# Kernel optimization log

Measured on AMD Instinct MI355X. Metric: run time of the kernel, lower is better.

Reference implementation:

```python
import jax, jax.numpy as jnp
import numpy as np

B, C, H, W = 4, 256, 64, 64
C8 = C // 8
MH, MW = 256, 256  # mask input resolution


def _conv(x, w, b, pad, dil=1):
    out = jax.lax.conv_general_dilated(
        x, w, window_strides=(1, 1),
        padding=[(pad, pad), (pad, pad)],
        rhs_dilation=(dil, dil),
        dimension_numbers=("NCHW", "OIHW", "NCHW"))
    return out + b[None, :, None, None]


def setup_inputs() -> dict:
    key = jax.random.key(0)
    ks = jax.random.split(key, 16)

    def w_init(k, shape):
        fan_in = shape[1] * shape[2] * shape[3]
        bound = 1.0 / np.sqrt(fan_in)
        return jax.random.uniform(k, shape, jnp.float32, -bound, bound)

    def b_init(k, n, fan_in):
        bound = 1.0 / np.sqrt(fan_in)
        return jax.random.uniform(k, (n,), jnp.float32, -bound, bound)

    return {
        "x": jax.random.normal(ks[0], (B, C, H, W), jnp.float32),
        "mask": jax.random.uniform(ks[1], (B, 1, MH, MW), jnp.float32),
        "w_ctx": w_init(ks[2], (C, C, 7, 7)),   "b_ctx": b_init(ks[3], C, C * 49),
        "w_wide": w_init(ks[4], (C, C, 5, 5)),  "b_wide": b_init(ks[5], C, C * 25),
        "w_comb": w_init(ks[6], (C, 2 * C, 1, 1)), "b_comb": b_init(ks[7], C, 2 * C),
        "w_q": w_init(ks[8], (C8, C, 1, 1)),    "b_q": b_init(ks[9], C8, C),
        "w_k": w_init(ks[10], (C8, C, 1, 1)),   "b_k": b_init(ks[11], C8, C),
        "w_v": w_init(ks[12], (C, C, 1, 1)),    "b_v": b_init(ks[13], C, C),
    }


def reference(x, mask, w_ctx, b_ctx, w_wide, b_wide, w_comb, b_comb,
              w_q, b_q, w_k, b_k, w_v, b_v):
    local_ctx = _conv(x, w_ctx, b_ctx, pad=3, dil=1)          # [B,C,H,W]
    wide_ctx = _conv(x, w_wide, b_wide, pad=6, dil=3)         # [B,C,H,W]
    multi = _conv(jnp.concatenate([local_ctx, wide_ctx], axis=1),
                  w_comb, b_comb, pad=0)                       # [B,C,H,W]

    b, c, h, w = multi.shape
    n = h * w
    q = _conv(multi, w_q, b_q, pad=0).reshape(b, C8, n)        # [B,C/8,N]
    k = _conv(multi, w_k, b_k, pad=0).reshape(b, C8, n)        # [B,C/8,N]
    v = _conv(multi, w_v, b_v, pad=0).reshape(b, c, n)         # [B,C,N]

    scores = jnp.einsum("bcm,bcn->bmn", q, k)                  # [B,N,N]
    attn = jax.nn.softmax(scores, axis=-1)
    out = jnp.einsum("bcn,bmn->bcm", v, attn).reshape(b, c, h, w)

    # nearest-neighbor resize of mask to (h, w), matching torch F.interpolate
    mh, mw = mask.shape[2], mask.shape[3]
    idx_h = (jnp.arange(h) * mh) // h
    idx_w = (jnp.arange(w) * mw) // w
    mask_r = mask[:, :, idx_h][:, :, :, idx_w]                 # [B,1,h,w]

    return out * (1.0 + mask_r)
```

## Files before the change

kernel.cpp:

```cpp
#include <hip/hip_runtime.h>
#include <math.h>

#define BB 4
#define CC 256
#define HH 64
#define WW 64
#define NN 4096

typedef _Float16 f16x8 __attribute__((ext_vector_type(8)));
typedef float f32x4 __attribute__((ext_vector_type(4)));

__global__ __launch_bounds__(256) void pad_kernel(
    const float* __restrict__ x, _Float16* __restrict__ xpad)
{
  int blk = blockIdx.x;
  int pr = blk % 76;
  int b  = blk / 76;
  int ci = threadIdx.x;
  int r = pr - 6;
  _Float16* dst = xpad + (((size_t)b*76 + pr)*76)*256 + ci;
  if (r < 0 || r >= HH) {
    for (int pc = 0; pc < 76; ++pc) dst[(size_t)pc*256] = (_Float16)0.f;
  } else {
    const float* src = x + ((size_t)b*CC + ci)*NN + (size_t)r*WW;
    for (int pc = 0; pc < 76; ++pc) {
      int c = pc - 6;
      float v = (c >= 0 && c < WW) ? src[c] : 0.f;
      dst[(size_t)pc*256] = (_Float16)v;
    }
  }
}

__global__ __launch_bounds__(256) void wcvt_kernel(
    const float* __restrict__ src, _Float16* __restrict__ dst, int T)
{
  int co = blockIdx.x;
  int ci = threadIdx.x;
  const float* s = src + ((size_t)co*256 + ci)*T;
  for (int t = 0; t < T; ++t)
    dst[(size_t)t*65536 + co*256 + ci] = (_Float16)s[t];
}

__global__ __launch_bounds__(256) void fcvt_kernel(
    const float* __restrict__ src, _Float16* __restrict__ dst, int n)
{
  int i = blockIdx.x * 256 + threadIdx.x;
  if (i < n) dst[i] = (_Float16)src[i];
}

template<int KS, int DIL>
__device__ __forceinline__ void conv_body(
    int blk, const _Float16* __restrict__ xpad, const _Float16* __restrict__ wb,
    const float* __restrict__ bias, _Float16* __restrict__ ctx_t, int c_off,
    char* xs)
{
  int ytile = blk & 31;
  int cot = (blk >> 5) & 1;
  int b = blk >> 6;
  int y0 = ytile * 2;
  int tid = threadIdx.x;
  int lane = tid & 63;
  int wv = tid >> 6;
  int wco = wv >> 1;
  int wsp = wv & 1;
  int l15 = lane & 15;
  int lg  = lane >> 4;

  f32x4 acc[2][4];
  #pragma unroll
  for (int m = 0; m < 2; ++m)
    #pragma unroll
    for (int n = 0; n < 4; ++n) acc[m][n] = (f32x4){0.f, 0.f, 0.f, 0.f};

  for (int kh = 0; kh < KS; ++kh) {
    int prow = 6 + y0 + (kh - KS/2) * DIL;
    const uint4* src = (const uint4*)(xpad + (((size_t)b*76 + prow)*76)*256);
    __syncthreads();
    #pragma unroll
    for (int i = 0; i < 10; ++i) {
      int ch = tid + i*512;
      if (ch < 4864) {
        uint4 v = src[ch];
        int r = ch >> 5, cq = ch & 31;
        *(uint4*)(xs + r*512 + ((cq << 4) ^ ((r & 7) << 4))) = v;
      }
    }
    __syncthreads();
    for (int kw = 0; kw < KS; ++kw) {
      int dx = (kw - KS/2) * DIL;
      int tap = kh*KS + kw;
      const _Float16* wt = wb + ((size_t)tap << 16)
                              + ((size_t)(cot*128 + wco*32 + l15) << 8) + (lg << 3);
      #pragma unroll
      for (int half = 0; half < 2; ++half) {
        f16x8 w0[4], w1[4];
        #pragma unroll
        for (int kq = 0; kq < 4; ++kq) {
          int ks = half*4 + kq;
          w0[kq] = *(const f16x8*)(wt + ks*32);
          w1[kq] = *(const f16x8*)(wt + 16*256 + ks*32);
        }
        #pragma unroll
        for (int kq = 0; kq < 4; ++kq) {
          int ks = half*4 + kq;
          #pragma unroll
          for (int nf = 0; nf < 4; ++nf) {
            int r = wsp*76 + 6 + nf*16 + l15 + dx;
            f16x8 bf = *(const f16x8*)(xs + r*512 + ((ks*64 + (lg << 4)) ^ ((r & 7) << 4)));
            acc[0][nf] = __builtin_amdgcn_mfma_f32_16x16x32_f16(w0[kq], bf, acc[0][nf], 0, 0, 0);
            acc[1][nf] = __builtin_amdgcn_mfma_f32_16x16x32_f16(w1[kq], bf, acc[1][nf], 0, 0, 0);
          }
        }
      }
    }
  }

  __syncthreads();
  _Float16* ep = (_Float16*)xs;
  #pragma unroll
  for (int m = 0; m < 2; ++m)
    #pragma unroll
    for (int i = 0; i < 4; ++i) {
      int co_l = wco*32 + m*16 + lg*4 + i;
      float bs = bias[cot*128 + co_l];
      #pragma unroll
      for (int nf = 0; nf < 4; ++nf) {
        int n_l = wsp*64 + nf*16 + l15;
        ep[n_l*136 + co_l] = (_Float16)(acc[m][nf][i] + bs);
      }
    }
  __syncthreads();
  const int cbase = c_off + cot*128;
  #pragma unroll
  for (int it = 0; it < 4; ++it) {
    int idx = tid + it*512;
    int n_l = idx >> 4, q = idx & 15;
    f16x8 val = *(const f16x8*)(ep + n_l*136 + q*8);
    *(f16x8*)(ctx_t + ((size_t)b*4096 + (size_t)y0*64 + n_l)*512 + cbase + q*8) = val;
  }
}

__global__ __launch_bounds__(512, 4) void conv_both_kernel(
    const _Float16* __restrict__ xpad,
    const _Float16* __restrict__ wb7, const _Float16* __restrict__ wb5,
    const float* __restrict__ b7, const float* __restrict__ b5,
    _Float16* __restrict__ ctx_t)
{
  __shared__ __align__(16) char xs[2*76*512];
  if (blockIdx.x < 256)
    conv_body<7, 1>(blockIdx.x, xpad, wb7, b7, ctx_t, 0, xs);
  else
    conv_body<5, 3>(blockIdx.x - 256, xpad, wb5, b5, ctx_t, 256, xs);
}

template<int K, int O, int BIASMODE>
__global__ __launch_bounds__(64) void gemm_nmajor_kernel(
    const _Float16* __restrict__ A, const _Float16* __restrict__ Wt,
    const float* __restrict__ bias0, const float* __restrict__ bias1,
    _Float16* __restrict__ outh)
{
  int nt = blockIdx.x;
  int ot = blockIdx.y;
  int lane = threadIdx.x;
  int l15 = lane & 15, lg = lane >> 4;
  int n0 = nt*64, o0 = ot*64;
  f32x4 acc[4][4] = {};
  for (int k0 = 0; k0 < K; k0 += 32) {
    f16x8 a[4], bfr[4];
    #pragma unroll
    for (int f = 0; f < 4; ++f)
      a[f] = *(const f16x8*)(A + (size_t)(n0 + f*16 + l15)*K + k0 + lg*8);
    #pragma unroll
    for (int f = 0; f < 4; ++f)
      bfr[f] = *(const f16x8*)(Wt + (size_t)(o0 + f*16 + l15)*K + k0 + lg*8);
    #pragma unroll
    for (int i = 0; i < 4; ++i)
      #pragma unroll
      for (int j = 0; j < 4; ++j)
        acc[i][j] = __builtin_amdgcn_mfma_f32_16x16x32_f16(a[i], bfr[j], acc[i][j], 0, 0, 0);
  }
  #pragma unroll
  for (int i = 0; i < 4; ++i)
    #pragma unroll
    for (int j = 0; j < 4; ++j)
      #pragma unroll
      for (int r = 0; r < 4; ++r) {
        int n = n0 + i*16 + lg*4 + r;
        int o = o0 + j*16 + l15;
        float bs = (BIASMODE == 0) ? bias0[o] : (o < 32 ? bias0[o] : bias1[o - 32]);
        outh[(size_t)n*O + o] = (_Float16)(acc[i][j][r] + bs);
      }
}

__global__ __launch_bounds__(64) void gemm_v_kernel(
    const _Float16* __restrict__ M, const _Float16* __restrict__ Wv,
    const float* __restrict__ bias, _Float16* __restrict__ v)
{
  int nt = blockIdx.x;
  int ct = blockIdx.y;
  int lane = threadIdx.x;
  int l15 = lane & 15, lg = lane >> 4;
  int n0 = nt*64, c0 = ct*64;
  f32x4 acc[4][4] = {};
  for (int k0 = 0; k0 < 256; k0 += 32) {
    f16x8 a[4], bfr[4];
    #pragma unroll
    for (int f = 0; f < 4; ++f)
      a[f] = *(const f16x8*)(Wv + (size_t)(c0 + f*16 + l15)*256 + k0 + lg*8);
    #pragma unroll
    for (int f = 0; f < 4; ++f)
      bfr[f] = *(const f16x8*)(M + (size_t)(n0 + f*16 + l15)*256 + k0 + lg*8);
    #pragma unroll
    for (int i = 0; i < 4; ++i)
      #pragma unroll
      for (int j = 0; j < 4; ++j)
        acc[i][j] = __builtin_amdgcn_mfma_f32_16x16x32_f16(a[i], bfr[j], acc[i][j], 0, 0, 0);
  }
  #pragma unroll
  for (int i = 0; i < 4; ++i)
    #pragma unroll
    for (int j = 0; j < 4; ++j)
      #pragma unroll
      for (int r = 0; r < 4; ++r) {
        int c = c0 + i*16 + lg*4 + r;
        int n_abs = n0 + j*16 + l15;
        int b = n_abs >> 12, n = n_abs & 4095;
        v[((size_t)(b*256 + c))*4096 + n] = (_Float16)(acc[i][j][r] + bias[c]);
      }
}

__global__ __launch_bounds__(256) void attn_stats_kernel(
    const _Float16* __restrict__ qh,
    float* __restrict__ rowmaxP, float* __restrict__ rowsumP)
{
  int blk = blockIdx.x;
  int b = blk >> 7, mt = (blk >> 1) & 63, nh = blk & 1;
  int tid = threadIdx.x, lane = tid & 63, w = tid >> 6;
  int l15 = lane & 15, lg = lane >> 4;
  size_t bN = (size_t)b * 4096;
  int mrow = mt*64 + w*16;
  f16x8 ah = *(const f16x8*)(qh + (bN + mrow + l15)*64 + lg*8);
  float rm[4] = {-3e38f, -3e38f, -3e38f, -3e38f};
  float sm[4] = {0.f, 0.f, 0.f, 0.f};
  for (int n0 = nh*2048; n0 < nh*2048 + 2048; n0 += 16) {
    f16x8 bh = *(const f16x8*)(qh + (bN + n0 + l15)*64 + 32 + lg*8);
    f32x4 s = {};
    s = __builtin_amdgcn_mfma_f32_16x16x32_f16(ah, bh, s, 0, 0, 0);
    #pragma unroll
    for (int i = 0; i < 4; ++i) {
      float nm = fmaxf(rm[i], s[i]);
      sm[i] = sm[i]*__expf(rm[i] - nm) + __expf(s[i] - nm);
      rm[i] = nm;
    }
  }
  #pragma unroll
  for (int off = 1; off <= 8; off <<= 1) {
    #pragma unroll
    for (int i = 0; i < 4; ++i) {
      float rmo = __shfl_xor(rm[i], off);
      float smo = __shfl_xor(sm[i], off);
      float M = fmaxf(rm[i], rmo);
      sm[i] = sm[i]*__expf(rm[i] - M) + smo*__expf(rmo - M);
      rm[i] = M;
    }
  }
  if (l15 == 0) {
    #pragma unroll
    for (int i = 0; i < 4; ++i) {
      size_t idx = (size_t)nh*16384 + bN + mrow + lg*4 + i;
      rowmaxP[idx] = rm[i];
      rowsumP[idx] = sm[i];
    }
  }
}

__global__ __launch_bounds__(512) void attn_out_kernel(
    const _Float16* __restrict__ qh, const _Float16* __restrict__ v,
    const float* __restrict__ rowmaxP, const float* __restrict__ rowsumP,
    const float* __restrict__ mask, float* __restrict__ out)
{
  __shared__ union U {
    struct { __align__(16) _Float16 vs[256*40]; __align__(16) _Float16 pl[64*40]; } s;
    float epi[256*68];
  } u;
  int blk = blockIdx.x;
  int b = blk >> 6, mt = blk & 63;
  int tid = threadIdx.x, lane = tid & 63, w = tid >> 6;
  int l15 = lane & 15, lg = lane >> 4;
  size_t bN = (size_t)b * 4096;
  int m0 = mt*64;

  int mf = w >> 1, nf2 = w & 1;
  f16x8 ah = *(const f16x8*)(qh + (bN + m0 + mf*16 + l15)*64 + lg*8);
  float rm[4], rsi[4];
  #pragma unroll
  for (int i = 0; i < 4; ++i) {
    size_t m = bN + m0 + mf*16 + lg*4 + i;
    float r0 = rowmaxP[m], r1 = rowmaxP[16384 + m];
    float s0 = rowsumP[m], s1 = rowsumP[16384 + m];
    float M = fmaxf(r0, r1);
    rm[i] = M;
    rsi[i] = 1.0f / (s0*__expf(r0 - M) + s1*__expf(r1 - M));
  }
  int mh = w >> 2, cw = (w & 3)*64;
  f32x4 acc[2][4] = {};
  const _Float16* vb = v + (size_t)b*256*4096;

  for (int n0 = 0; n0 < 4096; n0 += 32) {
    #pragma unroll
    for (int it = 0; it < 2; ++it) {
      int idx = tid + it*512;
      int c = idx >> 2, q = idx & 3;
      *(f16x8*)(u.s.vs + c*40 + q*8) = *(const f16x8*)(vb + (size_t)c*4096 + n0 + q*8);
    }
    {
      f16x8 bh = *(const f16x8*)(qh + (bN + n0 + nf2*16 + l15)*64 + 32 + lg*8);
      f32x4 s = {};
      s = __builtin_amdgcn_mfma_f32_16x16x32_f16(ah, bh, s, 0, 0, 0);
      #pragma unroll
      for (int i = 0; i < 4; ++i) {
        float p = __expf(s[i] - rm[i]) * rsi[i];
        u.s.pl[(mf*16 + lg*4 + i)*40 + nf2*16 + l15] = (_Float16)p;
      }
    }
    __syncthreads();
    {
      f16x8 pa[2], pb[4];
      #pragma unroll
      for (int af = 0; af < 2; ++af)
        pa[af] = *(const f16x8*)(u.s.pl + (mh*32 + af*16 + l15)*40 + lg*8);
      #pragma unroll
      for (int bf = 0; bf < 4; ++bf)
        pb[bf] = *(const f16x8*)(u.s.vs + (cw + bf*16 + l15)*40 + lg*8);
      #pragma unroll
      for (int af = 0; af < 2; ++af)
        #pragma unroll
        for (int bf = 0; bf < 4; ++bf)
          acc[af][bf] = __builtin_amdgcn_mfma_f32_16x16x32_f16(pa[af], pb[bf], acc[af][bf], 0, 0, 0);
    }
    __syncthreads();
  }

  #pragma unroll
  for (int af = 0; af < 2; ++af)
    #pragma unroll
    for (int bf = 0; bf < 4; ++bf)
      #pragma unroll
      for (int r = 0; r < 4; ++r) {
        int c = cw + bf*16 + l15;
        int ml = mh*32 + af*16 + lg*4 + r;
        u.epi[c*68 + ml] = acc[af][bf][r];
      }
  __syncthreads();
  const float* mb = mask + (size_t)b*65536 + (size_t)(mt*4)*256;
  #pragma unroll
  for (int it = 0; it < 8; ++it) {
    int idx = tid + it*512;
    int c = idx >> 4, q = idx & 15;
    f32x4 val = *(const f32x4*)(u.epi + c*68 + q*4);
    f32x4 o4;
    #pragma unroll
    for (int jj = 0; jj < 4; ++jj) {
      int xcol = q*4 + jj;
      o4[jj] = val[jj] * (1.0f + mb[xcol*4]);
    }
    *(f32x4*)(out + ((size_t)b*256 + c)*4096 + m0 + q*4) = o4;
  }
}

extern "C" void kernel_launch(void* const* d_in, const int* in_sizes, int n_in,
                              void* d_out, int out_size, void* d_ws, size_t ws_size,
                              hipStream_t stream)
{
  (void)in_sizes; (void)n_in; (void)out_size; (void)ws_size;
  const float* x      = (const float*)d_in[0];
  const float* mask   = (const float*)d_in[1];
  const float* w_ctx  = (const float*)d_in[2];
  const float* b_ctx  = (const float*)d_in[3];
  const float* w_wide = (const float*)d_in[4];
  const float* b_wide = (const float*)d_in[5];
  const float* w_comb = (const float*)d_in[6];
  const float* b_comb = (const float*)d_in[7];
  const float* w_q    = (const float*)d_in[8];
  const float* b_q    = (const float*)d_in[9];
  const float* w_k    = (const float*)d_in[10];
  const float* b_k    = (const float*)d_in[11];
  const float* w_v    = (const float*)d_in[12];
  const float* b_v    = (const float*)d_in[13];
  float* out = (float*)d_out;

  float* ws = (float*)d_ws;
  _Float16* xpad    = (_Float16*)(ws);
  _Float16* wb7     = (_Float16*)(ws + 2957312);
  _Float16* wb5     = (_Float16*)(ws + 4562944);
  _Float16* ctx_t   = (_Float16*)(ws + 5382144);
  _Float16* wcombH  = (_Float16*)(ws + 9576448);
  _Float16* wqkH    = (_Float16*)(ws + 9641984);
  _Float16* wvH     = (_Float16*)(ws + 9650176);
  _Float16* multi_t = (_Float16*)(ws);
  _Float16* qkt_h   = (_Float16*)(ws + 2097152);
  float*    rowmaxP = ws + 2621440;
  float*    rowsumP = ws + 2654208;
  _Float16* vbuf    = (_Float16*)(ws + 5382144);

  pad_kernel<<<BB*76, 256, 0, stream>>>(x, xpad);
  wcvt_kernel<<<256, 256, 0, stream>>>(w_ctx, wb7, 49);
  wcvt_kernel<<<256, 256, 0, stream>>>(w_wide, wb5, 25);
  fcvt_kernel<<<512, 256, 0, stream>>>(w_comb, wcombH, 131072);
  fcvt_kernel<<<32, 256, 0, stream>>>(w_q, wqkH, 8192);
  fcvt_kernel<<<32, 256, 0, stream>>>(w_k, wqkH + 8192, 8192);
  fcvt_kernel<<<256, 256, 0, stream>>>(w_v, wvH, 65536);

  conv_both_kernel<<<512, 512, 0, stream>>>(xpad, wb7, wb5, b_ctx, b_wide, ctx_t);

  gemm_nmajor_kernel<512, 256, 0><<<dim3(256, 4), 64, 0, stream>>>(
      ctx_t, wcombH, b_comb, nullptr, multi_t);
  gemm_nmajor_kernel<256, 64, 1><<<dim3(256, 1), 64, 0, stream>>>(
      multi_t, wqkH, b_q, b_k, qkt_h);
  gemm_v_kernel<<<dim3(256, 4), 64, 0, stream>>>(multi_t, wvH, b_v, vbuf);

  attn_stats_kernel<<<512, 256, 0, stream>>>(qkt_h, rowmaxP, rowsumP);
  attn_out_kernel<<<256, 512, 0, stream>>>(qkt_h, vbuf, rowmaxP, rowsumP,
                                           mask, out);
}
```

Before: 528.0 us.

## Split conv reduction dimension across wave halves with larger per-wave MFMA tiles

Reorganizes the conv warp layout so each wave computes a 64x64 output tile (4x4 MFMA fragments) over half of the input-channel range, with two wave groups splitting K and reducing partial sums through fp32 shared memory in the epilogue. This raises register-level reuse of weight and activation fragments per MFMA, cutting LDS and global weight loads per FLOP. It costs more accumulator registers (64 floats per lane), which may hurt occupancy under the 512x4 launch bound, and adds an extra shared-memory reduction pass with fp32 staging.

```diff
diff --git a/kernel.cpp b/kernel.cpp
--- a/kernel.cpp
+++ b/kernel.cpp
@@ -8,6 +8,7 @@
 #define NN 4096
 
 typedef _Float16 f16x8 __attribute__((ext_vector_type(8)));
+typedef _Float16 f16x4 __attribute__((ext_vector_type(4)));
 typedef float f32x4 __attribute__((ext_vector_type(4)));
 
 __global__ __launch_bounds__(256) void pad_kernel(
@@ -61,16 +62,17 @@
   int tid = threadIdx.x;
   int lane = tid & 63;
   int wv = tid >> 6;
-  int wco = wv >> 1;
-  int wsp = wv & 1;
+  int wco = wv & 1;
+  int wsp = (wv >> 1) & 1;
+  int khf = wv >> 2;
   int l15 = lane & 15;
   int lg  = lane >> 4;
 
-  f32x4 acc[2][4];
-  #pragma unroll
-  for (int m = 0; m < 2; ++m)
-    #pragma unroll
-    for (int n = 0; n < 4; ++n) acc[m][n] = (f32x4){0.f, 0.f, 0.f, 0.f};
+  f32x4 acc[4][4];
+  #pragma unroll
+  for (int i = 0; i < 4; ++i)
+    #pragma unroll
+    for (int j = 0; j < 4; ++j) acc[i][j] = (f32x4){0.f, 0.f, 0.f, 0.f};
 
   for (int kh = 0; kh < KS; ++kh) {
     int prow = 6 + y0 + (kh - KS/2) * DIL;
@@ -90,53 +92,69 @@
       int dx = (kw - KS/2) * DIL;
       int tap = kh*KS + kw;
       const _Float16* wt = wb + ((size_t)tap << 16)
-                              + ((size_t)(cot*128 + wco*32 + l15) << 8) + (lg << 3);
-      #pragma unroll
-      for (int half = 0; half < 2; ++half) {
-        f16x8 w0[4], w1[4];
-        #pragma unroll
-        for (int kq = 0; kq < 4; ++kq) {
-          int ks = half*4 + kq;
-          w0[kq] = *(const f16x8*)(wt + ks*32);
-          w1[kq] = *(const f16x8*)(wt + 16*256 + ks*32);
+                              + ((size_t)(cot*128 + wco*64 + l15) << 8)
+                              + khf*128 + (lg << 3);
+      #pragma unroll
+      for (int kq = 0; kq < 4; ++kq) {
+        int ks = khf*4 + kq;
+        f16x8 wa[4], bf[4];
+        #pragma unroll
+        for (int jA = 0; jA < 4; ++jA)
+          wa[jA] = *(const f16x8*)(wt + jA*4096 + kq*32);
+        #pragma unroll
+        for (int nf = 0; nf < 4; ++nf) {
+          int r = wsp*76 + 6 + nf*16 + l15 + dx;
+          bf[nf] = *(const f16x8*)(xs + r*512 + ((ks*64 + (lg << 4)) ^ ((r & 7) << 4)));
         }
         #pragma unroll
-        for (int kq = 0; kq < 4; ++kq) {
-          int ks = half*4 + kq;
+        for (int jA = 0; jA < 4; ++jA)
           #pragma unroll
-          for (int nf = 0; nf < 4; ++nf) {
-            int r = wsp*76 + 6 + nf*16 + l15 + dx;
-            f16x8 bf = *(const f16x8*)(xs + r*512 + ((ks*64 + (lg << 4)) ^ ((r & 7) << 4)));
-            acc[0][nf] = __builtin_amdgcn_mfma_f32_16x16x32_f16(w0[kq], bf, acc[0][nf], 0, 0, 0);
-            acc[1][nf] = __builtin_amdgcn_mfma_f32_16x16x32_f16(w1[kq], bf, acc[1][nf], 0, 0, 0);
-          }
+          for (int nf = 0; nf < 4; ++nf)
+            acc[jA][nf] = __builtin_amdgcn_mfma_f32_16x16x32_f16(wa[jA], bf[nf], acc[jA][nf], 0, 0, 0);
+      }
+    }
+  }
+
+  float* epf = (float*)xs;
+  __syncthreads();
+  if (khf == 1) {
+    #pragma unroll
+    for (int jA = 0; jA < 4; ++jA)
+      #pragma unroll
+      for (int nf = 0; nf < 4; ++nf)
+        #pragma unroll
+        for (int r = 0; r < 4; ++r) {
+          int n_l = wsp*64 + nf*16 + l15;
+          int co_l = wco*64 + jA*16 + lg*4 + r;
+          epf[n_l*136 + co_l] = acc[jA][nf][r];
         }
-      }
-    }
-  }
-
+  }
   __syncthreads();
-  _Float16* ep = (_Float16*)xs;
-  #pragma unroll
-  for (int m = 0; m < 2; ++m)
-    #pragma unroll
-    for (int i = 0; i < 4; ++i) {
-      int co_l = wco*32 + m*16 + lg*4 + i;
-      float bs = bias[cot*128 + co_l];
-      #pragma unroll
-      for (int nf = 0; nf < 4; ++nf) {
-        int n_l = wsp*64 + nf*16 + l15;
-        ep[n_l*136 + co_l] = (_Float16)(acc[m][nf][i] + bs);
-      }
-    }
+  if (khf == 0) {
+    #pragma unroll
+    for (int jA = 0; jA < 4; ++jA)
+      #pragma unroll
+      for (int r = 0; r < 4; ++r) {
+        int co_l = wco*64 + jA*16 + lg*4 + r;
+        float bs = bias[cot*128 + co_l];
+        #pragma unroll
+        for (int nf = 0; nf < 4; ++nf) {
+          int n_l = wsp*64 + nf*16 + l15;
+          epf[n_l*136 + co_l] += acc[jA][nf][r] + bs;
+        }
+      }
+  }
   __syncthreads();
   const int cbase = c_off + cot*128;
   #pragma unroll
-  for (int it = 0; it < 4; ++it) {
+  for (int it = 0; it < 8; ++it) {
     int idx = tid + it*512;
-    int n_l = idx >> 4, q = idx & 15;
-    f16x8 val = *(const f16x8*)(ep + n_l*136 + q*8);
-    *(f16x8*)(ctx_t + ((size_t)b*4096 + (size_t)y0*64 + n_l)*512 + cbase + q*8) = val;
+    int n_l = idx >> 5, q = idx & 31;
+    f32x4 v4 = *(const f32x4*)(epf + n_l*136 + q*4);
+    f16x4 h4;
+    #pragma unroll
+    for (int j = 0; j < 4; ++j) h4[j] = (_Float16)v4[j];
+    *(f16x4*)(ctx_t + ((size_t)b*4096 + (size_t)y0*64 + n_l)*512 + cbase + q*4) = h4;
   }
 }
 
```

After: 557.2 us. 5.5% more time.
